# Kernel tuning notes

Measured on AMD Instinct MI355X. Metric: run time of the kernel, lower is better.

Reference implementation:

```python
import jax, jax.numpy as jnp
import numpy as np

SIGMA = 1.0
ALPHA = 1.5
EPS = 1e-08
N, D = 8192, 128


def setup_inputs() -> dict:
    key = jax.random.key(0)
    k1, k2 = jax.random.split(key)
    z1 = jax.random.normal(k1, (N, D), dtype=jnp.float32)
    z2 = jax.random.normal(k2, (N, D), dtype=jnp.float32)
    return {"z1": z1, "z2": z2}


def _l2_normalize(x, eps=1e-12):
    # matches F.normalize(x, dim=1): x / max(||x||, eps)
    n = jnp.linalg.norm(x, axis=1, keepdims=True)
    return x / jnp.maximum(n, eps)


def _f_prime(u):
    # KL divergence: f'(u) = log(u + eps) + 1
    return jnp.log(u + EPS) + 1.0


def _f_star(t):
    # KL divergence conjugate: f*(t) = exp(t - 1)
    return jnp.exp(t - 1.0)


def reference(z1, z2):
    z1 = _l2_normalize(z1)
    z2 = _l2_normalize(z2)
    n = z1.shape[0]

    # positive term: ||z1_i - z2_i||^2 per row
    d_pos = jnp.sum((z1 - z2) ** 2, axis=1)                       # (N,)
    g_pos = jnp.exp(-d_pos / (2.0 * SIGMA ** 2))
    s_pos = _f_prime(g_pos)

    # negative term: squared pairwise distances within z1 (N x N)
    sq = jnp.sum(z1 * z1, axis=1)                                  # (N,)
    d2 = sq[:, None] + sq[None, :] - 2.0 * (z1 @ z1.T)             # (N, N)
    d2 = jnp.maximum(d2, 0.0)
    g_neg = jnp.exp(-d2 / (2.0 * SIGMA ** 2))
    s_neg = _f_prime(g_neg)
    star_neg = _f_star(s_neg)

    # masked mean over off-diagonal entries (N*(N-1) of them)
    off_diag = 1.0 - jnp.eye(n, dtype=star_neg.dtype)
    star_mean = jnp.sum(star_neg * off_diag) / (n * (n - 1))

    loss = -jnp.mean(s_pos) + ALPHA * star_mean
    return loss
```

## Files before the change

kernel.cpp:

```cpp
#include <hip/hip_runtime.h>

#define NROWS 8192
#define DIM 128
#define NT 32
#define NPAIRBLK (NT * (NT + 1) / 2)

typedef _Float16 f16x8 __attribute__((ext_vector_type(8)));
typedef _Float16 f16x2 __attribute__((ext_vector_type(2)));
typedef float f32x16 __attribute__((ext_vector_type(16)));

#define L2E 1.4426950408889634f

#define AS1(p) ((const __attribute__((address_space(1))) void*)(p))
#define AS3(p) ((__attribute__((address_space(3))) void*)(p))

__global__ __launch_bounds__(1024) void fmicl_normalize(
    const float* __restrict__ z1, const float* __restrict__ z2,
    _Float16* __restrict__ zh, float* __restrict__ sposB) {
  const int wid = threadIdx.x >> 6;
  const int lane = threadIdx.x & 63;
  const int row = blockIdx.x * 16 + wid;
  const float2 a = ((const float2*)(z1 + (size_t)row * DIM))[lane];
  const float2 b = ((const float2*)(z2 + (size_t)row * DIM))[lane];
  float s1 = a.x * a.x + a.y * a.y;
  float s2 = b.x * b.x + b.y * b.y;
#pragma unroll
  for (int off = 32; off; off >>= 1) {
    s1 += __shfl_xor(s1, off);
    s2 += __shfl_xor(s2, off);
  }
  const float inv1 = 1.0f / fmaxf(sqrtf(s1), 1e-12f);
  const float inv2 = 1.0f / fmaxf(sqrtf(s2), 1e-12f);
  const float n1x = a.x * inv1, n1y = a.y * inv1;
  const float n2x = b.x * inv2, n2y = b.y * inv2;
  const float dx = n1x - n2x, dy = n1y - n2y;
  float dp = dx * dx + dy * dy;
#pragma unroll
  for (int off = 32; off; off >>= 1) dp += __shfl_xor(dp, off);
  f16x2 h;
  h.x = (_Float16)n1x;
  h.y = (_Float16)n1y;
  *(f16x2*)(zh + (size_t)row * DIM + 2 * lane) = h;
  __shared__ float sposL[16];
  if (lane == 0)
    sposL[wid] = logf(expf(-0.5f * dp) + 1e-8f) + 1.0f;
  __syncthreads();
  if (threadIdx.x == 0) {
    float s = 0.0f;
#pragma unroll
    for (int k = 0; k < 16; ++k) s += sposL[k];
    sposB[blockIdx.x] = s;
  }
}

__global__ __launch_bounds__(1024, 4) void fmicl_pairwise(
    const _Float16* __restrict__ zh, float* __restrict__ pairP) {
  __shared__ _Float16 S[512 * DIM];
  __shared__ float wsum[16];

  const int tid = threadIdx.x;
  const int bid = blockIdx.x;

  int rt = (int)(32.5f - sqrtf(32.5f * 32.5f - 2.0f * (float)bid));
  if (rt < 0) rt = 0;
  while (rt > 0 && (rt * NT - (rt * (rt - 1)) / 2) > bid) --rt;
  while (((rt + 1) * NT - ((rt + 1) * rt) / 2) <= bid) ++rt;
  const int ct = rt + (bid - (rt * NT - (rt * (rt - 1)) / 2));

  const int lane = tid & 63;
  const int wid = tid >> 6;
  const int i0 = rt << 8;
  const int j0 = ct << 8;

#pragma unroll
  for (int t = 0; t < 8; ++t) {
    const int P = t * 16 + wid;
    const int R = P * 4 + (lane >> 4);
    const int csrc = (lane & 15) ^ (R & 15);
    const _Float16* srow = (R < 256) ? zh + (size_t)(i0 + R) * DIM
                                     : zh + (size_t)(j0 + R - 256) * DIM;
    __builtin_amdgcn_global_load_lds(AS1(srow + csrc * 8), AS3(S + P * 512),
                                     16, 0, 0);
  }
  __syncthreads();

  const int l31 = lane & 31;
  const int lhi = lane >> 5;
  const int wm = (wid >> 2) * 64;
  const int wn = (wid & 3) * 64;
  const uint4* S4 = (const uint4*)S;
  const int ra0 = wm + l31;
  const int ra1 = wm + 32 + l31;
  const int rb0 = 256 + wn + l31;
  const int rb1 = 256 + wn + 32 + l31;
  f32x16 acc00 = {}, acc01 = {}, acc10 = {}, acc11 = {};
#pragma unroll
  for (int ks = 0; ks < 8; ++ks) {
    const int kg = ks * 2 + lhi;
    const uint4 va0 = S4[ra0 * 16 + (kg ^ (ra0 & 15))];
    const uint4 va1 = S4[ra1 * 16 + (kg ^ (ra1 & 15))];
    const uint4 vb0 = S4[rb0 * 16 + (kg ^ (rb0 & 15))];
    const uint4 vb1 = S4[rb1 * 16 + (kg ^ (rb1 & 15))];
    const f16x8 a0 = __builtin_bit_cast(f16x8, va0);
    const f16x8 a1 = __builtin_bit_cast(f16x8, va1);
    const f16x8 b0 = __builtin_bit_cast(f16x8, vb0);
    const f16x8 b1 = __builtin_bit_cast(f16x8, vb1);
    acc00 = __builtin_amdgcn_mfma_f32_32x32x16_f16(a0, b0, acc00, 0, 0, 0);
    acc01 = __builtin_amdgcn_mfma_f32_32x32x16_f16(a0, b1, acc01, 0, 0, 0);
    acc10 = __builtin_amdgcn_mfma_f32_32x32x16_f16(a1, b0, acc10, 0, 0, 0);
    acc11 = __builtin_amdgcn_mfma_f32_32x32x16_f16(a1, b1, acc11, 0, 0, 0);
  }

  float gsum = 0.0f;
#pragma unroll
  for (int mi = 0; mi < 2; ++mi) {
#pragma unroll
    for (int ni = 0; ni < 2; ++ni) {
      const f32x16& acc = (mi == 0) ? (ni == 0 ? acc00 : acc01)
                                    : (ni == 0 ? acc10 : acc11);
      const bool diagsub =
          (rt == ct) && (wm + mi * 32 == wn + ni * 32);
      if (diagsub) {
#pragma unroll
        for (int r = 0; r < 16; ++r) {
          const float e =
              __builtin_amdgcn_exp2f(fmaf(L2E, acc[r], -L2E));
          const int mloc = (r & 3) + 4 * lhi + 8 * (r >> 2);
          gsum += (mloc != l31) ? e : 0.0f;
        }
      } else {
#pragma unroll
        for (int r = 0; r < 16; ++r)
          gsum += __builtin_amdgcn_exp2f(fmaf(L2E, acc[r], -L2E));
      }
    }
  }
#pragma unroll
  for (int off = 32; off; off >>= 1) gsum += __shfl_xor(gsum, off);
  if (lane == 0) wsum[wid] = gsum;
  __syncthreads();
  if (tid == 0) {
    float s = 0.0f;
#pragma unroll
    for (int k = 0; k < 16; ++k) s += wsum[k];
    pairP[bid] = (rt == ct) ? s : 2.0f * s;
  }
}

__global__ void fmicl_reduce(const float* __restrict__ pairP,
                             const float* __restrict__ sposB,
                             float* __restrict__ out) {
  const int t = threadIdx.x;
  double nsum = (t < NPAIRBLK) ? (double)pairP[t] : 0.0;
  double psum = (t < 512) ? (double)sposB[t] : 0.0;
#pragma unroll
  for (int off = 32; off; off >>= 1) {
    nsum += __shfl_xor(nsum, off);
    psum += __shfl_xor(psum, off);
  }
  __shared__ double ls[2][16];
  const int lane = t & 63;
  const int wid = t >> 6;
  if (lane == 0) {
    ls[0][wid] = nsum;
    ls[1][wid] = psum;
  }
  __syncthreads();
  if (t == 0) {
    double n = 0.0, p = 0.0;
#pragma unroll
    for (int k = 0; k < 16; ++k) {
      n += ls[0][k];
      p += ls[1][k];
    }
    const double pos_mean = p / (double)NROWS;
    const double star_mean = n / ((double)NROWS * (double)(NROWS - 1)) + 1e-8;
    out[0] = (float)(-pos_mean + 1.5 * star_mean);
  }
}

extern "C" void kernel_launch(void* const* d_in, const int* in_sizes, int n_in,
                              void* d_out, int out_size, void* d_ws,
                              size_t ws_size, hipStream_t stream) {
  const float* z1 = (const float*)d_in[0];
  const float* z2 = (const float*)d_in[1];
  float* out = (float*)d_out;
  char* ws = (char*)d_ws;

  float* pairP = (float*)(ws + 0);
  float* sposB = (float*)(ws + 4096);
  _Float16* zh = (_Float16*)(ws + 6144);

  fmicl_normalize<<<512, 1024, 0, stream>>>(z1, z2, zh, sposB);
  fmicl_pairwise<<<NPAIRBLK, 1024, 0, stream>>>(zh, pairP);
  fmicl_reduce<<<1, 1024, 0, stream>>>(pairP, sposB, out);
}
```

Baseline: 30.95 us.

## Shrink pairwise tiles to 128x128 and interleave tile order across blocks

Halves the pairwise tile edge from 256 to 128 rows. That gives 2080 triangular tiles instead of 528, processed by 512-thread blocks with half the LDS each. A block-index permutation spreads consecutive blocks across strided tiles, which should balance work across XCDs and raise occupancy. The trade-off is lower data reuse per tile, meaning more global and LDS traffic per FLOP, plus more per-block reduction overhead. The final reduce kernel and workspace offsets are adjusted for the larger partial-sum array.

New measurement: 30.13 us. -2.7%, faster.

```diff
diff --git a/kernel.cpp b/kernel.cpp
--- a/kernel.cpp
+++ b/kernel.cpp
@@ -2,7 +2,7 @@
 
 #define NROWS 8192
 #define DIM 128
-#define NT 32
+#define NT 64
 #define NPAIRBLK (NT * (NT + 1) / 2)
 
 typedef _Float16 f16x8 __attribute__((ext_vector_type(8)));
@@ -53,32 +53,32 @@
   }
 }
 
-__global__ __launch_bounds__(1024, 4) void fmicl_pairwise(
+__global__ __launch_bounds__(512, 4) void fmicl_pairwise(
     const _Float16* __restrict__ zh, float* __restrict__ pairP) {
-  __shared__ _Float16 S[512 * DIM];
-  __shared__ float wsum[16];
+  __shared__ _Float16 S[256 * DIM];
+  __shared__ float wsum[8];
 
   const int tid = threadIdx.x;
-  const int bid = blockIdx.x;
+  const int tile = (blockIdx.x & 7) * (NPAIRBLK / 8) + (blockIdx.x >> 3);
 
-  int rt = (int)(32.5f - sqrtf(32.5f * 32.5f - 2.0f * (float)bid));
+  int rt = (int)(64.5f - sqrtf(64.5f * 64.5f - 2.0f * (float)tile));
   if (rt < 0) rt = 0;
-  while (rt > 0 && (rt * NT - (rt * (rt - 1)) / 2) > bid) --rt;
-  while (((rt + 1) * NT - ((rt + 1) * rt) / 2) <= bid) ++rt;
-  const int ct = rt + (bid - (rt * NT - (rt * (rt - 1)) / 2));
+  while (rt > 0 && (rt * NT - (rt * (rt - 1)) / 2) > tile) --rt;
+  while (((rt + 1) * NT - ((rt + 1) * rt) / 2) <= tile) ++rt;
+  const int ct = rt + (tile - (rt * NT - (rt * (rt - 1)) / 2));
 
   const int lane = tid & 63;
   const int wid = tid >> 6;
-  const int i0 = rt << 8;
-  const int j0 = ct << 8;
+  const int i0 = rt << 7;
+  const int j0 = ct << 7;
 
 #pragma unroll
   for (int t = 0; t < 8; ++t) {
-    const int P = t * 16 + wid;
+    const int P = t * 8 + wid;
     const int R = P * 4 + (lane >> 4);
     const int csrc = (lane & 15) ^ (R & 15);
-    const _Float16* srow = (R < 256) ? zh + (size_t)(i0 + R) * DIM
-                                     : zh + (size_t)(j0 + R - 256) * DIM;
+    const _Float16* srow = (R < 128) ? zh + (size_t)(i0 + R) * DIM
+                                     : zh + (size_t)(j0 + R - 128) * DIM;
     __builtin_amdgcn_global_load_lds(AS1(srow + csrc * 8), AS3(S + P * 512),
                                      16, 0, 0);
   }
@@ -86,53 +86,42 @@
 
   const int l31 = lane & 31;
   const int lhi = lane >> 5;
-  const int wm = (wid >> 2) * 64;
-  const int wn = (wid & 3) * 64;
+  const int wm = (wid >> 1) * 32;
+  const int wn = (wid & 1) * 64;
   const uint4* S4 = (const uint4*)S;
-  const int ra0 = wm + l31;
-  const int ra1 = wm + 32 + l31;
-  const int rb0 = 256 + wn + l31;
-  const int rb1 = 256 + wn + 32 + l31;
-  f32x16 acc00 = {}, acc01 = {}, acc10 = {}, acc11 = {};
+  const int ra = wm + l31;
+  const int rb0 = 128 + wn + l31;
+  const int rb1 = 128 + wn + 32 + l31;
+  f32x16 acc0 = {}, acc1 = {};
 #pragma unroll
   for (int ks = 0; ks < 8; ++ks) {
     const int kg = ks * 2 + lhi;
-    const uint4 va0 = S4[ra0 * 16 + (kg ^ (ra0 & 15))];
-    const uint4 va1 = S4[ra1 * 16 + (kg ^ (ra1 & 15))];
+    const uint4 va = S4[ra * 16 + (kg ^ (ra & 15))];
     const uint4 vb0 = S4[rb0 * 16 + (kg ^ (rb0 & 15))];
     const uint4 vb1 = S4[rb1 * 16 + (kg ^ (rb1 & 15))];
-    const f16x8 a0 = __builtin_bit_cast(f16x8, va0);
-    const f16x8 a1 = __builtin_bit_cast(f16x8, va1);
-    const f16x8 b0 = __builtin_bit_cast(f16x8, vb0);
-    const f16x8 b1 = __builtin_bit_cast(f16x8, vb1);
-    acc00 = __builtin_amdgcn_mfma_f32_32x32x16_f16(a0, b0, acc00, 0, 0, 0);
-    acc01 = __builtin_amdgcn_mfma_f32_32x32x16_f16(a0, b1, acc01, 0, 0, 0);
-    acc10 = __builtin_amdgcn_mfma_f32_32x32x16_f16(a1, b0, acc10, 0, 0, 0);
-    acc11 = __builtin_amdgcn_mfma_f32_32x32x16_f16(a1, b1, acc11, 0, 0, 0);
+    const f16x8 af = __builtin_bit_cast(f16x8, va);
+    acc0 = __builtin_amdgcn_mfma_f32_32x32x16_f16(
+        af, __builtin_bit_cast(f16x8, vb0), acc0, 0, 0, 0);
+    acc1 = __builtin_amdgcn_mfma_f32_32x32x16_f16(
+        af, __builtin_bit_cast(f16x8, vb1), acc1, 0, 0, 0);
   }
 
   float gsum = 0.0f;
 #pragma unroll
-  for (int mi = 0; mi < 2; ++mi) {
+  for (int ni = 0; ni < 2; ++ni) {
+    const f32x16& acc = ni ? acc1 : acc0;
+    const bool diagsub = (rt == ct) && (wm == wn + ni * 32);
+    if (diagsub) {
 #pragma unroll
-    for (int ni = 0; ni < 2; ++ni) {
-      const f32x16& acc = (mi == 0) ? (ni == 0 ? acc00 : acc01)
-                                    : (ni == 0 ? acc10 : acc11);
-      const bool diagsub =
-          (rt == ct) && (wm + mi * 32 == wn + ni * 32);
-      if (diagsub) {
+      for (int r = 0; r < 16; ++r) {
+        const float e = __builtin_amdgcn_exp2f(fmaf(L2E, acc[r], -L2E));
+        const int mloc = (r & 3) + 4 * lhi + 8 * (r >> 2);
+        gsum += (mloc != l31) ? e : 0.0f;
+      }
+    } else {
 #pragma unroll
-        for (int r = 0; r < 16; ++r) {
-          const float e =
-              __builtin_amdgcn_exp2f(fmaf(L2E, acc[r], -L2E));
-          const int mloc = (r & 3) + 4 * lhi + 8 * (r >> 2);
-          gsum += (mloc != l31) ? e : 0.0f;
-        }
-      } else {
-#pragma unroll
-        for (int r = 0; r < 16; ++r)
-          gsum += __builtin_amdgcn_exp2f(fmaf(L2E, acc[r], -L2E));
-      }
+      for (int r = 0; r < 16; ++r)
+        gsum += __builtin_amdgcn_exp2f(fmaf(L2E, acc[r], -L2E));
     }
   }
 #pragma unroll
@@ -142,8 +131,8 @@
   if (tid == 0) {
     float s = 0.0f;
 #pragma unroll
-    for (int k = 0; k < 16; ++k) s += wsum[k];
-    pairP[bid] = (rt == ct) ? s : 2.0f * s;
+    for (int k = 0; k < 8; ++k) s += wsum[k];
+    pairP[tile] = (rt == ct) ? s : 2.0f * s;
   }
 }
 
@@ -151,7 +140,8 @@
                              const float* __restrict__ sposB,
                              float* __restrict__ out) {
   const int t = threadIdx.x;
-  double nsum = (t < NPAIRBLK) ? (double)pairP[t] : 0.0;
+  double nsum = (double)pairP[t] + (double)pairP[t + 1024];
+  if (t < NPAIRBLK - 2048) nsum += (double)pairP[t + 2048];
   double psum = (t < 512) ? (double)sposB[t] : 0.0;
 #pragma unroll
   for (int off = 32; off; off >>= 1) {
@@ -188,10 +178,10 @@
   char* ws = (char*)d_ws;
 
   float* pairP = (float*)(ws + 0);
-  float* sposB = (float*)(ws + 4096);
-  _Float16* zh = (_Float16*)(ws + 6144);
+  float* sposB = (float*)(ws + 8448);
+  _Float16* zh = (_Float16*)(ws + 10496);
 
   fmicl_normalize<<<512, 1024, 0, stream>>>(z1, z2, zh, sposB);
-  fmicl_pairwise<<<NPAIRBLK, 1024, 0, stream>>>(zh, pairP);
+  fmicl_pairwise<<<NPAIRBLK, 512, 0, stream>>>(zh, pairP);
   fmicl_reduce<<<1, 1024, 0, stream>>>(pairP, sposB, out);
 }
```
